# Kernel tuning notes

Hardware: AMD Instinct MI355X
Metric: run time of the kernel (lower is better)

Reference implementation:

```python
import jax, jax.numpy as jnp
import numpy as np

XB = (-51.2, 51.2, 0.8); YB = (-51.2, 51.2, 0.8); ZB = (-10.0, 10.0, 20.0); DB = (4.0, 45.0, 1.0)
H_FEAT, W_FEAT = 16, 44
C_IN, C_OUT = 512, 64
D = int((DB[1] - DB[0]) / DB[2])  # 41
DX = np.array([XB[2], YB[2], ZB[2]], np.float32)
BX = np.array([XB[0] + XB[2] / 2.0, YB[0] + YB[2] / 2.0, ZB[0] + ZB[2] / 2.0], np.float32)
NX0 = int((XB[1] - XB[0]) / XB[2])  # 128
NX1 = int((YB[1] - YB[0]) / YB[2])  # 128
NX2 = int((ZB[1] - ZB[0]) / ZB[2])  # 1
NVOX = NX0 * NX1 * NX2


def _frustum():
    ds = np.arange(DB[0], DB[1], DB[2], dtype=np.float32)[:, None, None]
    xs = np.linspace(0, W_FEAT - 1, W_FEAT, dtype=np.float32)[None, None, :]
    ys = np.linspace(0, H_FEAT - 1, H_FEAT, dtype=np.float32)[None, :, None]
    shape = (D, H_FEAT, W_FEAT)
    return jnp.asarray(np.stack([np.broadcast_to(xs, shape), np.broadcast_to(ys, shape), np.broadcast_to(ds, shape)], -1))


def setup_inputs() -> dict:
    rng = np.random.default_rng(0)
    B, N = 4, 6
    img_feats = rng.standard_normal((B, N, C_IN, H_FEAT, W_FEAT)).astype(np.float32)
    depth_w = (0.02 * rng.standard_normal((D + C_OUT, C_IN))).astype(np.float32)
    depth_b = np.zeros((D + C_OUT,), np.float32)
    ang = rng.uniform(-np.pi, np.pi, (B, N))
    c, s = np.cos(ang), np.sin(ang)
    rots = np.zeros((B, N, 3, 3), np.float32)
    rots[..., 0, 0] = c; rots[..., 0, 1] = -s
    rots[..., 1, 0] = s; rots[..., 1, 1] = c
    rots[..., 2, 2] = 1.0
    trans = rng.uniform(-2.0, 2.0, (B, N, 3)).astype(np.float32)
    trans[..., 2] *= 0.25
    intr = np.array([[20.0, 0.0, 22.0], [0.0, 20.0, 8.0], [0.0, 0.0, 1.0]], np.float32)
    intrins = np.broadcast_to(intr, (B, N, 3, 3)).copy()
    post_rots = np.broadcast_to(np.eye(3, dtype=np.float32), (B, N, 3, 3)).copy()
    post_trans = np.zeros((B, N, 3), np.float32)
    return {k: jnp.asarray(v) for k, v in dict(img_feats=img_feats, depth_w=depth_w, depth_b=depth_b, rots=rots, trans=trans, intrins=intrins, post_rots=post_rots, post_trans=post_trans).items()}


def reference(img_feats, depth_w, depth_b, rots, trans, intrins, post_rots, post_trans):
    B, N = img_feats.shape[:2]
    # depth net: 1x1 conv == channel matmul
    xf = img_feats.reshape(B * N, C_IN, H_FEAT, W_FEAT)
    feat = jnp.einsum('bchw,oc->bohw', xf, depth_w) + depth_b[None, :, None, None]
    depth = jax.nn.softmax(feat[:, :D], axis=1)      # (BN, D, H, W)
    tran = feat[:, D:]                               # (BN, C, H, W)
    # lift: outer product over depth x channel
    outer = depth[:, None, :, :, :] * tran[:, :, None, :, :]          # (BN, C, D, H, W)
    feats = outer.reshape(B, N, C_OUT, D, H_FEAT, W_FEAT).transpose(0, 1, 3, 4, 5, 2)  # (B,N,D,H,W,C)
    # geometry
    pts = _frustum()[None, None] - post_trans[:, :, None, None, None, :]
    pts = jnp.einsum('bnij,bndhwj->bndhwi', jnp.linalg.inv(post_rots), pts)
    pts = jnp.concatenate([pts[..., :2] * pts[..., 2:3], pts[..., 2:3]], axis=-1)
    combine = rots @ jnp.linalg.inv(intrins)
    pts = jnp.einsum('bnij,bndhwj->bndhwi', combine, pts) + trans[:, :, None, None, None, :]
    # voxelize; int cast truncates toward zero, matching torch .long()
    coords = ((pts - jnp.asarray(BX)) / jnp.asarray(DX)).astype(jnp.int32)  # (B,N,D,H,W,3)
    cx, cy, cz = coords[..., 0], coords[..., 1], coords[..., 2]
    valid = (cx >= 0) & (cx < NX0) & (cy >= 0) & (cy < NX1) & (cz >= 0) & (cz < NX2)
    ranks = jnp.where(valid, cx + cy * NX0 + cz * (NX0 * NX1), NVOX)  # invalid -> dropped bin
    sums = jax.ops.segment_sum(feats.reshape(-1, C_OUT), ranks.reshape(-1), num_segments=NVOX + 1)
    bev = sums[:NVOX].reshape(NX2, NX1, NX0, C_OUT).sum(0)            # (ny, nx, C)
    return jnp.transpose(bev, (2, 0, 1))[None]                        # (1, C, ny, nx)
```

## Files before the change

kernel.cpp:

```cpp
#include <hip/hip_runtime.h>
#include <cmath>

#define CIN   512
#define COUT  64
#define DBINS 41
#define NFEAT 105
#define HF    16
#define WF    44
#define NPIX  704
#define NCAM  24
#define NXG   128
#define NVOX  16384
#define ROWF  210
#define BEVOF 146
#define NPAIR (NCAM * NPIX * DBINS)
#define NSUB  16
#define NCNT  (NVOX * NSUB)


#define WS_BSUM  5120
#define WS_BBASE 6144
#define WS_FEAT  8192
#define WS_OFFS  14200832
#define WS_REC   15249408
#define WS_CNT   15249408

__device__ __forceinline__ void inv3(const double a[9], double o[9]) {
    double c00 =  a[4]*a[8] - a[5]*a[7];
    double c01 = -(a[3]*a[8] - a[5]*a[6]);
    double c02 =  a[3]*a[7] - a[4]*a[6];
    double det = a[0]*c00 + a[1]*c01 + a[2]*c02;
    double id  = 1.0 / det;
    o[0] = c00 * id;
    o[1] = -(a[1]*a[8] - a[2]*a[7]) * id;
    o[2] =  (a[1]*a[5] - a[2]*a[4]) * id;
    o[3] = c01 * id;
    o[4] =  (a[0]*a[8] - a[2]*a[6]) * id;
    o[5] = -(a[0]*a[5] - a[2]*a[3]) * id;
    o[6] = c02 * id;
    o[7] = -(a[0]*a[7] - a[1]*a[6]) * id;
    o[8] =  (a[0]*a[4] - a[1]*a[3]) * id;
}

__global__ void setup_cams_k(const float* __restrict__ rots,
                             const float* __restrict__ trans,
                             const float* __restrict__ intrins,
                             const float* __restrict__ post_rots,
                             const float* __restrict__ post_trans,
                             double* __restrict__ cams) {
    int i = blockIdx.x * blockDim.x + threadIdx.x;
    if (i >= NCAM) return;
    double R[9], K[9], PR[9], Kinv[9], PRinv[9];
    for (int k = 0; k < 9; ++k) {
        R[k]  = (double)rots[i*9 + k];
        K[k]  = (double)intrins[i*9 + k];
        PR[k] = (double)post_rots[i*9 + k];
    }
    inv3(K, Kinv);
    inv3(PR, PRinv);
    double* o = cams + (size_t)i * 24;
    for (int k = 0; k < 9; ++k) o[k] = PRinv[k];
    o[9]  = (double)post_trans[i*3 + 0];
    o[10] = (double)post_trans[i*3 + 1];
    o[11] = (double)post_trans[i*3 + 2];
    for (int r = 0; r < 3; ++r)
        for (int c = 0; c < 3; ++c)
            o[12 + r*3 + c] = R[r*3+0]*Kinv[0*3+c] + R[r*3+1]*Kinv[1*3+c] + R[r*3+2]*Kinv[2*3+c];
    o[21] = (double)trans[i*3 + 0];
    o[22] = (double)trans[i*3 + 1];
    o[23] = (double)trans[i*3 + 2];
}

__global__ __launch_bounds__(512) void gemm_feat_k(const float* __restrict__ x,
                                                   const float* __restrict__ w,
                                                   const float* __restrict__ bias,
                                                   float* __restrict__ feat) {
    __shared__ float smem[4352];

    int bx   = blockIdx.x;
    int kh   = bx & 1;
    int oh   = (bx >> 1) & 3;
    int tile = bx >> 3;
    int p0g  = tile * 128;
    int lane = threadIdx.x & 63;
    int wid  = threadIdx.x >> 6;
    int obase0 = (oh < 3) ? oh * 32 : 73;

    int og = obase0 + wid * 4;
    const float* wbase = w + (size_t)__builtin_amdgcn_readfirstlane(og) * CIN + kh * 256;

    int spx  = threadIdx.x & 127;
    int skq  = threadIdx.x >> 7;
    int gpix = p0g + spx;
    int sbn  = gpix / NPIX;
    int sp   = gpix - sbn * NPIX;
    const float* gx = x + ((size_t)sbn * CIN + kh * 256) * NPIX + sp;

    float xr[4];
    float acc[4][2];
    #pragma unroll
    for (int i = 0; i < 4; ++i)
        #pragma unroll
        for (int j = 0; j < 2; ++j) acc[i][j] = 0.0f;

    #pragma unroll
    for (int c = 0; c < 4; ++c)
        xr[c] = gx[(size_t)(skq * 4 + c) * NPIX];
    *reinterpret_cast<float4*>(&smem[(skq * 128 + spx) * 4]) =
        make_float4(xr[0], xr[1], xr[2], xr[3]);
    #pragma unroll
    for (int c = 0; c < 4; ++c)
        xr[c] = gx[(size_t)(16 + skq * 4 + c) * NPIX];
    __syncthreads();

    #pragma unroll 1
    for (int kt = 0; kt < 16; ++kt) {
        int cur = kt & 1;
        if (kt < 15) {
            float* xsn = smem + (cur ^ 1) * 2048;
            *reinterpret_cast<float4*>(&xsn[(skq * 128 + spx) * 4]) =
                make_float4(xr[0], xr[1], xr[2], xr[3]);
        }
        if (kt < 14) {
            #pragma unroll
            for (int c = 0; c < 4; ++c)
                xr[c] = gx[(size_t)((kt + 2) * 16 + skq * 4 + c) * NPIX];
        }
        const float* xs = smem + cur * 2048;
        const float* wk = wbase + kt * 16;
        #pragma unroll
        for (int kq = 0; kq < 4; ++kq) {
            float4 xv[2];
            #pragma unroll
            for (int j = 0; j < 2; ++j)
                xv[j] = *reinterpret_cast<const float4*>(&xs[(kq * 128 + lane + j * 64) * 4]);
            #pragma unroll
            for (int i = 0; i < 4; ++i) {
                float4 wv = *reinterpret_cast<const float4*>(wk + (size_t)i * CIN + (kq << 2));
                #pragma unroll
                for (int j = 0; j < 2; ++j) {
                    acc[i][j] = fmaf(xv[j].x, wv.x, acc[i][j]);
                    acc[i][j] = fmaf(xv[j].y, wv.y, acc[i][j]);
                    acc[i][j] = fmaf(xv[j].z, wv.z, acc[i][j]);
                    acc[i][j] = fmaf(xv[j].w, wv.w, acc[i][j]);
                }
            }
        }
        __syncthreads();
    }

    float* ep = smem;
    #pragma unroll
    for (int i = 0; i < 4; ++i) {
        int o = obase0 + wid * 4 + i;
        float b = (kh == 0) ? bias[o] : 0.0f;
        #pragma unroll
        for (int j = 0; j < 2; ++j)
            ep[(lane + j * 64) * 33 + wid * 4 + i] = acc[i][j] + b;
    }
    __syncthreads();
    for (int idx = threadIdx.x; idx < 128 * 32; idx += 512) {
        int px = idx >> 5;
        int ol = idx & 31;
        feat[(size_t)(p0g + px) * ROWF + kh * NFEAT + obase0 + ol] = ep[px * 33 + ol];
    }
}

__global__ __launch_bounds__(256) void phaseA_k(float* __restrict__ feat,
                                                const double* __restrict__ cams,
                                                int* __restrict__ cnt16) {
    int wid  = threadIdx.x >> 6;
    int lane = threadIdx.x & 63;
    int pix  = blockIdx.x * 4 + wid;
    int bn   = pix / NPIX;
    int p    = pix - bn * NPIX;
    int h    = p / WF;
    int wpx  = p - h * WF;

    __shared__ float f[4][NFEAT];
    float* row = feat + (size_t)pix * ROWF;
    for (int o = lane; o < NFEAT; o += 64) f[wid][o] = row[o] + row[NFEAT + o];
    __syncthreads();

    float v = (lane < DBINS) ? f[wid][lane] : -1e30f;
    float m = v;
    #pragma unroll
    for (int o = 32; o > 0; o >>= 1) m = fmaxf(m, __shfl_xor(m, o, 64));
    float e = (lane < DBINS) ? expf(v - m) : 0.0f;
    float s = e;
    #pragma unroll
    for (int o = 32; o > 0; o >>= 1) s += __shfl_xor(s, o, 64);

    if (lane < DBINS) {
        float pd = e / s;
        const double* cm = cams + (size_t)bn * 24;
        double dd = 4.0 + (double)lane;
        double ax = (double)wpx - cm[9];
        double ay = (double)h   - cm[10];
        double az = dd          - cm[11];
        double q0 = cm[0]*ax + cm[1]*ay + cm[2]*az;
        double q1 = cm[3]*ax + cm[4]*ay + cm[5]*az;
        double q2 = cm[6]*ax + cm[7]*ay + cm[8]*az;
        double r0 = q0 * q2, r1 = q1 * q2, r2 = q2;
        double sx = cm[12]*r0 + cm[13]*r1 + cm[14]*r2 + cm[21];
        double sy = cm[15]*r0 + cm[16]*r1 + cm[17]*r2 + cm[22];
        double sz = cm[18]*r0 + cm[19]*r1 + cm[20]*r2 + cm[23];
        int cx = (int)((sx + 50.8) / 0.8);
        int cy = (int)((sy + 50.8) / 0.8);
        int cz = (int)(sz / 20.0);
        bool ok = (cx >= 0) && (cx < NXG) && (cy >= 0) && (cy < NXG) && (cz == 0);
        int rk = ok ? (cy * NXG + cx) : -1;
        row[64 + lane] = pd;
        ((int*)row)[105 + lane] = rk;
        if (rk >= 0) atomicAdd(&cnt16[(pix & 15) * NVOX + rk], 1);
    }
    row[lane] = f[wid][DBINS + lane];
    row[BEVOF + lane] = 0.0f;
}

__device__ __forceinline__ int physidx(int l) { return (l & 15) * NVOX + (l >> 4); }

__global__ __launch_bounds__(256) void scan1_k(const int* __restrict__ cnt,
                                               int* __restrict__ bsum) {
    __shared__ int sc[256];
    int t = threadIdx.x;
    int base = blockIdx.x * 1024 + t * 4;
    int s = 0;
    #pragma unroll
    for (int j = 0; j < 4; ++j) s += cnt[physidx(base + j)];
    sc[t] = s;
    __syncthreads();
    for (int off = 128; off > 0; off >>= 1) {
        if (t < off) sc[t] += sc[t + off];
        __syncthreads();
    }
    if (t == 0) bsum[blockIdx.x] = sc[0];
}

__global__ __launch_bounds__(256) void scan2_k(const int* __restrict__ bsum,
                                               int* __restrict__ bbase) {
    __shared__ int sc[256];
    int t = threadIdx.x;
    int v = bsum[t];
    sc[t] = v;
    __syncthreads();
    for (int off = 1; off < 256; off <<= 1) {
        int a = (t >= off) ? sc[t - off] : 0;
        __syncthreads();
        sc[t] += a;
        __syncthreads();
    }
    bbase[t] = sc[t] - v;
}

__global__ __launch_bounds__(256) void scan3_k(const int* __restrict__ cnt,
                                               const int* __restrict__ bbase,
                                               int* __restrict__ offs) {
    __shared__ int sc[256];
    int t = threadIdx.x;
    int base = blockIdx.x * 1024 + t * 4;
    int loc[4];
    int s = 0;
    #pragma unroll
    for (int j = 0; j < 4; ++j) { loc[j] = cnt[physidx(base + j)]; s += loc[j]; }
    sc[t] = s;
    __syncthreads();
    for (int off = 1; off < 256; off <<= 1) {
        int a = (t >= off) ? sc[t - off] : 0;
        __syncthreads();
        sc[t] += a;
        __syncthreads();
    }
    int run = bbase[blockIdx.x] + sc[t] - s;
    #pragma unroll
    for (int j = 0; j < 4; ++j) { offs[physidx(base + j)] = run; run += loc[j]; }
}

__global__ __launch_bounds__(256) void place_k(const float* __restrict__ feat,
                                               int* __restrict__ offs16,
                                               unsigned* __restrict__ rec) {
    int i = blockIdx.x * 256 + threadIdx.x;
    if (i >= NPAIR) return;
    int pix = i / DBINS;
    int d   = i - pix * DBINS;
    const int* rowI = (const int*)(feat + (size_t)pix * ROWF);
    int r = rowI[105 + d];
    if (r >= 0) {
        int pos = atomicAdd(&offs16[(pix & 15) * NVOX + r], 1);
        rec[pos] = ((unsigned)pix << 6) | (unsigned)d;
    }
}

__global__ __launch_bounds__(256) void combine_k(float* __restrict__ feat,
                                                 const int* __restrict__ offs16,
                                                 const unsigned* __restrict__ rec) {
    int ncnt = offs16[NCNT - 1];
    int lane = threadIdx.x & 63;
    int wave = (blockIdx.x << 2) + (threadIdx.x >> 6);
    int nwav = gridDim.x << 2;
    int nchunk = (ncnt + 31) >> 5;

    for (int ch = wave; ch < nchunk; ch += nwav) {
        int i0 = ch << 5;
        int n  = min(32, ncnt - i0);
        int   rv = -1, pv = 0;
        float wv = 0.0f;
        if (lane < n) {
            unsigned e = rec[i0 + lane];
            pv = (int)(e >> 6);
            int d = (int)(e & 63u);
            const float* row = feat + (size_t)pv * ROWF;
            rv = ((const int*)row)[105 + d];
            wv = row[64 + d];
        }
        float acc = 0.0f;
        if (n == 32) {
            float xv[32];
            #pragma unroll
            for (int j = 0; j < 32; ++j) {
                int pj = __shfl(pv, j, 64);
                xv[j] = feat[(size_t)pj * ROWF + lane];
            }
            #pragma unroll
            for (int j = 0; j < 32; ++j) {
                int   rj = __shfl(rv, j, 64);
                float wj = __shfl(wv, j, 64);
                acc = fmaf(wj, xv[j], acc);
                int rn = __shfl(rv, (j + 1) & 31, 64);
                if (j == 31 || rn != rj) {
                    atomicAdd(&feat[(size_t)rj * ROWF + BEVOF + lane], acc);
                    acc = 0.0f;
                }
            }
        } else {
            for (int j = 0; j < n; ++j) {
                int   rj = __shfl(rv, j, 64);
                float wj = __shfl(wv, j, 64);
                int   pj = __shfl(pv, j, 64);
                acc = fmaf(wj, feat[(size_t)pj * ROWF + lane], acc);
                int rn = __shfl(rv, (j + 1) & 31, 64);
                if (j == n - 1 || rn != rj) {
                    atomicAdd(&feat[(size_t)rj * ROWF + BEVOF + lane], acc);
                    acc = 0.0f;
                }
            }
        }
    }
}

__global__ __launch_bounds__(256) void transpose_k(const float* __restrict__ feat,
                                                   float* __restrict__ out) {
    __shared__ float t[64][65];
    int r0 = blockIdx.x * 64;
    int c  = threadIdx.x & 63;
    int r4 = threadIdx.x >> 6;
    #pragma unroll
    for (int i = 0; i < 16; ++i) {
        int r = r4 + i * 4;
        t[r][c] = feat[(size_t)(r0 + r) * ROWF + BEVOF + c];
    }
    __syncthreads();
    int rl  = threadIdx.x & 63;
    int cc0 = threadIdx.x >> 6;
    #pragma unroll
    for (int i = 0; i < 16; ++i) {
        int ch = cc0 + i * 4;
        out[(size_t)ch * NVOX + r0 + rl] = t[rl][ch];
    }
}

extern "C" void kernel_launch(void* const* d_in, const int* in_sizes, int n_in,
                              void* d_out, int out_size, void* d_ws, size_t ws_size,
                              hipStream_t stream) {
    const float* img   = (const float*)d_in[0];
    const float* dw    = (const float*)d_in[1];
    const float* db    = (const float*)d_in[2];
    const float* rots  = (const float*)d_in[3];
    const float* trans = (const float*)d_in[4];
    const float* intr  = (const float*)d_in[5];
    const float* prot  = (const float*)d_in[6];
    const float* ptrn  = (const float*)d_in[7];
    float* out = (float*)d_out;

    char* ws = (char*)d_ws;
    double*   cams   = (double*)ws;
    int*      bsum   = (int*)(ws + WS_BSUM);
    int*      bbase  = (int*)(ws + WS_BBASE);
    float*    feat   = (float*)(ws + WS_FEAT);
    int*      offs16 = (int*)(ws + WS_OFFS);
    unsigned* rec    = (unsigned*)(ws + WS_REC);
    int*      cnt16  = (int*)(ws + WS_CNT);

    hipMemsetAsync(cnt16, 0, NCNT * sizeof(int), stream);
    setup_cams_k<<<1, 64, 0, stream>>>(rots, trans, intr, prot, ptrn, cams);
    gemm_feat_k<<<1056, 512, 0, stream>>>(img, dw, db, feat);
    phaseA_k<<<NCAM * NPIX / 4, 256, 0, stream>>>(feat, cams, cnt16);
    scan1_k<<<256, 256, 0, stream>>>(cnt16, bsum);
    scan2_k<<<1, 256, 0, stream>>>(bsum, bbase);
    scan3_k<<<256, 256, 0, stream>>>(cnt16, bbase, offs16);
    place_k<<<(NPAIR + 255) / 256, 256, 0, stream>>>(feat, offs16, rec);
    combine_k<<<3072, 256, 0, stream>>>(feat, offs16, rec);
    transpose_k<<<NVOX / 64, 256, 0, stream>>>(feat, out);
}
```

Before: 116.3 us.

## Fold count zeroing into setup kernel and shrink GEMM output tile to 16 channels

```diff
diff --git a/kernel.cpp b/kernel.cpp
--- a/kernel.cpp
+++ b/kernel.cpp
@@ -42,49 +42,57 @@
     o[8] =  (a[0]*a[4] - a[1]*a[3]) * id;
 }
 
-__global__ void setup_cams_k(const float* __restrict__ rots,
-                             const float* __restrict__ trans,
-                             const float* __restrict__ intrins,
-                             const float* __restrict__ post_rots,
-                             const float* __restrict__ post_trans,
-                             double* __restrict__ cams) {
-    int i = blockIdx.x * blockDim.x + threadIdx.x;
-    if (i >= NCAM) return;
-    double R[9], K[9], PR[9], Kinv[9], PRinv[9];
-    for (int k = 0; k < 9; ++k) {
-        R[k]  = (double)rots[i*9 + k];
-        K[k]  = (double)intrins[i*9 + k];
-        PR[k] = (double)post_rots[i*9 + k];
-    }
-    inv3(K, Kinv);
-    inv3(PR, PRinv);
-    double* o = cams + (size_t)i * 24;
-    for (int k = 0; k < 9; ++k) o[k] = PRinv[k];
-    o[9]  = (double)post_trans[i*3 + 0];
-    o[10] = (double)post_trans[i*3 + 1];
-    o[11] = (double)post_trans[i*3 + 2];
-    for (int r = 0; r < 3; ++r)
-        for (int c = 0; c < 3; ++c)
-            o[12 + r*3 + c] = R[r*3+0]*Kinv[0*3+c] + R[r*3+1]*Kinv[1*3+c] + R[r*3+2]*Kinv[2*3+c];
-    o[21] = (double)trans[i*3 + 0];
-    o[22] = (double)trans[i*3 + 1];
-    o[23] = (double)trans[i*3 + 2];
-}
-
-__global__ __launch_bounds__(512) void gemm_feat_k(const float* __restrict__ x,
+__global__ __launch_bounds__(64) void setup_zero_k(const float* __restrict__ rots,
+                                                   const float* __restrict__ trans,
+                                                   const float* __restrict__ intrins,
+                                                   const float* __restrict__ post_rots,
+                                                   const float* __restrict__ post_trans,
+                                                   double* __restrict__ cams,
+                                                   int* __restrict__ cnt16) {
+    int base = (blockIdx.x * 64 + threadIdx.x) * 16;
+    int4 z = make_int4(0, 0, 0, 0);
+    #pragma unroll
+    for (int j = 0; j < 4; ++j)
+        *reinterpret_cast<int4*>(&cnt16[base + j * 4]) = z;
+
+    if (blockIdx.x == 0 && threadIdx.x < NCAM) {
+        int i = threadIdx.x;
+        double R[9], K[9], PR[9], Kinv[9], PRinv[9];
+        for (int k = 0; k < 9; ++k) {
+            R[k]  = (double)rots[i*9 + k];
+            K[k]  = (double)intrins[i*9 + k];
+            PR[k] = (double)post_rots[i*9 + k];
+        }
+        inv3(K, Kinv);
+        inv3(PR, PRinv);
+        double* o = cams + (size_t)i * 24;
+        for (int k = 0; k < 9; ++k) o[k] = PRinv[k];
+        o[9]  = (double)post_trans[i*3 + 0];
+        o[10] = (double)post_trans[i*3 + 1];
+        o[11] = (double)post_trans[i*3 + 2];
+        for (int r = 0; r < 3; ++r)
+            for (int c = 0; c < 3; ++c)
+                o[12 + r*3 + c] = R[r*3+0]*Kinv[0*3+c] + R[r*3+1]*Kinv[1*3+c] + R[r*3+2]*Kinv[2*3+c];
+        o[21] = (double)trans[i*3 + 0];
+        o[22] = (double)trans[i*3 + 1];
+        o[23] = (double)trans[i*3 + 2];
+    }
+}
+
+__global__ __launch_bounds__(256) void gemm_feat_k(const float* __restrict__ x,
                                                    const float* __restrict__ w,
                                                    const float* __restrict__ bias,
                                                    float* __restrict__ feat) {
-    __shared__ float smem[4352];
+    __shared__ float smem[4096];
 
     int bx   = blockIdx.x;
     int kh   = bx & 1;
-    int oh   = (bx >> 1) & 3;
-    int tile = bx >> 3;
+    int oh   = (bx >> 1) % 7;
+    int tile = (bx >> 1) / 7;
     int p0g  = tile * 128;
     int lane = threadIdx.x & 63;
     int wid  = threadIdx.x >> 6;
-    int obase0 = (oh < 3) ? oh * 32 : 73;
+    int obase0 = (oh < 6) ? oh * 16 : 89;
 
     int og = obase0 + wid * 4;
     const float* wbase = w + (size_t)__builtin_amdgcn_readfirstlane(og) * CIN + kh * 256;
@@ -96,7 +104,7 @@
     int sp   = gpix - sbn * NPIX;
     const float* gx = x + ((size_t)sbn * CIN + kh * 256) * NPIX + sp;
 
-    float xr[4];
+    float xr[2][4];
     float acc[4][2];
     #pragma unroll
     for (int i = 0; i < 4; ++i)
@@ -104,13 +112,19 @@
         for (int j = 0; j < 2; ++j) acc[i][j] = 0.0f;
 
     #pragma unroll
-    for (int c = 0; c < 4; ++c)
-        xr[c] = gx[(size_t)(skq * 4 + c) * NPIX];
-    *reinterpret_cast<float4*>(&smem[(skq * 128 + spx) * 4]) =
-        make_float4(xr[0], xr[1], xr[2], xr[3]);
-    #pragma unroll
-    for (int c = 0; c < 4; ++c)
-        xr[c] = gx[(size_t)(16 + skq * 4 + c) * NPIX];
+    for (int q = 0; q < 2; ++q)
+        #pragma unroll
+        for (int c = 0; c < 4; ++c)
+            xr[q][c] = gx[(size_t)((skq + 2 * q) * 4 + c) * NPIX];
+    #pragma unroll
+    for (int q = 0; q < 2; ++q)
+        *reinterpret_cast<float4*>(&smem[((skq + 2 * q) * 128 + spx) * 4]) =
+            make_float4(xr[q][0], xr[q][1], xr[q][2], xr[q][3]);
+    #pragma unroll
+    for (int q = 0; q < 2; ++q)
+        #pragma unroll
+        for (int c = 0; c < 4; ++c)
+            xr[q][c] = gx[(size_t)(16 + (skq + 2 * q) * 4 + c) * NPIX];
     __syncthreads();
 
     #pragma unroll 1
@@ -118,13 +132,17 @@
         int cur = kt & 1;
         if (kt < 15) {
             float* xsn = smem + (cur ^ 1) * 2048;
-            *reinterpret_cast<float4*>(&xsn[(skq * 128 + spx) * 4]) =
-                make_float4(xr[0], xr[1], xr[2], xr[3]);
+            #pragma unroll
+            for (int q = 0; q < 2; ++q)
+                *reinterpret_cast<float4*>(&xsn[((skq + 2 * q) * 128 + spx) * 4]) =
+                    make_float4(xr[q][0], xr[q][1], xr[q][2], xr[q][3]);
         }
         if (kt < 14) {
             #pragma unroll
-            for (int c = 0; c < 4; ++c)
-                xr[c] = gx[(size_t)((kt + 2) * 16 + skq * 4 + c) * NPIX];
+            for (int q = 0; q < 2; ++q)
+                #pragma unroll
+                for (int c = 0; c < 4; ++c)
+                    xr[q][c] = gx[(size_t)((kt + 2) * 16 + (skq + 2 * q) * 4 + c) * NPIX];
         }
         const float* xs = smem + cur * 2048;
         const float* wk = wbase + kt * 16;
@@ -156,13 +174,13 @@
         float b = (kh == 0) ? bias[o] : 0.0f;
         #pragma unroll
         for (int j = 0; j < 2; ++j)
-            ep[(lane + j * 64) * 33 + wid * 4 + i] = acc[i][j] + b;
-    }
-    __syncthreads();
-    for (int idx = threadIdx.x; idx < 128 * 32; idx += 512) {
-        int px = idx >> 5;
-        int ol = idx & 31;
-        feat[(size_t)(p0g + px) * ROWF + kh * NFEAT + obase0 + ol] = ep[px * 33 + ol];
+            ep[(lane + j * 64) * 17 + wid * 4 + i] = acc[i][j] + b;
+    }
+    __syncthreads();
+    for (int idx = threadIdx.x; idx < 128 * 16; idx += 256) {
+        int px = idx >> 4;
+        int ol = idx & 15;
+        feat[(size_t)(p0g + px) * ROWF + kh * NFEAT + obase0 + ol] = ep[px * 17 + ol];
     }
 }
 
@@ -391,9 +409,8 @@
     unsigned* rec    = (unsigned*)(ws + WS_REC);
     int*      cnt16  = (int*)(ws + WS_CNT);
 
-    hipMemsetAsync(cnt16, 0, NCNT * sizeof(int), stream);
-    setup_cams_k<<<1, 64, 0, stream>>>(rots, trans, intr, prot, ptrn, cams);
-    gemm_feat_k<<<1056, 512, 0, stream>>>(img, dw, db, feat);
+    setup_zero_k<<<256, 64, 0, stream>>>(rots, trans, intr, prot, ptrn, cams, cnt16);
+    gemm_feat_k<<<1848, 256, 0, stream>>>(img, dw, db, feat);
     phaseA_k<<<NCAM * NPIX / 4, 256, 0, stream>>>(feat, cams, cnt16);
     scan1_k<<<256, 256, 0, stream>>>(cnt16, bsum);
     scan2_k<<<1, 256, 0, stream>>>(bsum, bbase);
```

New measurement: 114.0 us. Within noise of the previous version (-2.0%).
